# Kernel tuning notes

Hardware: AMD Instinct MI355X
Metric: run time of the kernel (lower is better)

## Reference

```python
import jax, jax.numpy as jnp
import numpy as np

NUM_GROUPS = 8
NUM_HEADS = 4
EPS = 1e-5


def group_norm(x, w, b):
    # x: [B, C, H, W]; normalize over (C/G, H, W) within each of G groups
    B, C, H, W = x.shape
    xg = x.reshape(B, NUM_GROUPS, C // NUM_GROUPS, H, W)
    mean = xg.mean(axis=(2, 3, 4), keepdims=True)
    var = xg.var(axis=(2, 3, 4), keepdims=True)
    xn = ((xg - mean) * jax.lax.rsqrt(var + EPS)).reshape(B, C, H, W)
    return xn * w[None, :, None, None] + b[None, :, None, None]


def setup_inputs() -> dict:
    key = jax.random.key(0)
    ks = jax.random.split(key, 7)
    B, C, H, W = 4, 256, 64, 64
    x = jax.random.normal(ks[0], (B, C, H, W), dtype=jnp.float32)
    gn_w = jax.random.normal(ks[1], (C,), dtype=jnp.float32) * 0.1 + 1.0
    gn_b = jax.random.normal(ks[2], (C,), dtype=jnp.float32) * 0.1
    qkv_w = jax.random.normal(ks[3], (3 * C, C), dtype=jnp.float32) / np.sqrt(C)
    qkv_b = jax.random.normal(ks[4], (3 * C,), dtype=jnp.float32) * 0.02
    proj_w = jax.random.normal(ks[5], (C, C), dtype=jnp.float32) / np.sqrt(C)
    proj_b = jax.random.normal(ks[6], (C,), dtype=jnp.float32) * 0.02
    return {"x": x, "gn_w": gn_w, "gn_b": gn_b, "qkv_w": qkv_w,
            "qkv_b": qkv_b, "proj_w": proj_w, "proj_b": proj_b}


def reference(x, gn_w, gn_b, qkv_w, qkv_b, proj_w, proj_b):
    B, C, H, W = x.shape
    nh = NUM_HEADS
    hd = C // nh
    scale = hd ** -0.5
    N = H * W

    h = group_norm(x, gn_w, gn_b)
    # 1x1 conv == channel matmul: [B, 3C, H, W]
    qkv = jnp.einsum('oc,bchw->bohw', qkv_w, h) + qkv_b[None, :, None, None]
    qkv = qkv.reshape(B, 3, nh, hd, N)  # matches torch .view(B,3,nh,hd,HW)
    q, k, v = qkv[:, 0], qkv[:, 1], qkv[:, 2]  # each [B, nh, hd, N]

    attn = jnp.einsum('bhdn,bhdm->bhnm', q, k) * scale  # [B, nh, N, N]
    attn = jax.nn.softmax(attn, axis=-1)
    out = jnp.einsum('bhnm,bhdm->bhdn', attn, v)  # [B, nh, hd, N]
    out = out.reshape(B, C, H, W)

    proj = jnp.einsum('oc,bchw->bohw', proj_w, out) + proj_b[None, :, None, None]
    return x + proj
```

## Files before the change

### kernel.cpp

```cpp
#include <hip/hip_runtime.h>
#include <hip/hip_bf16.h>

#define BB   4
#define CC   256
#define NN   4096
#define NH   4
#define HD   64
#define NG   8
#define GSZ  32
#define EPSV 1e-5f
#define SCALE_L2E 0.18033688f

typedef __bf16 bf16x8 __attribute__((ext_vector_type(8)));
typedef float  f32x4  __attribute__((ext_vector_type(4)));

#define MFMA16(a, b, c)  __builtin_amdgcn_mfma_f32_16x16x32_bf16((a), (b), (c), 0, 0, 0)

#if __has_builtin(__builtin_amdgcn_exp2f)
#define EXP2F __builtin_amdgcn_exp2f
#else
#define EXP2F exp2f
#endif

#define WAITV(n)  asm volatile("s_waitcnt vmcnt(" #n ")" ::: "memory")
#define WAITL0    asm volatile("s_waitcnt lgkmcnt(0)" ::: "memory")
#define SBAR      __builtin_amdgcn_s_barrier()
#define SCHED0    __builtin_amdgcn_sched_barrier(0)

__device__ inline unsigned short f2bf(float f) {
    unsigned int u = __float_as_uint(f);
    u += 0x7fffu + ((u >> 16) & 1u);
    return (unsigned short)(u >> 16);
}

__device__ __forceinline__ bf16x8 pk8(const f32x4& p0, const f32x4& p1) {
    alignas(16) unsigned int u[4];
    u[0] = __builtin_amdgcn_perm(__float_as_uint(p0[1]), __float_as_uint(p0[0]), 0x07060302u);
    u[1] = __builtin_amdgcn_perm(__float_as_uint(p0[3]), __float_as_uint(p0[2]), 0x07060302u);
    u[2] = __builtin_amdgcn_perm(__float_as_uint(p1[1]), __float_as_uint(p1[0]), 0x07060302u);
    u[3] = __builtin_amdgcn_perm(__float_as_uint(p1[3]), __float_as_uint(p1[2]), 0x07060302u);
    return *reinterpret_cast<bf16x8*>(u);
}

__device__ __forceinline__ void async_ld16(void* lds, const void* g) {
    __builtin_amdgcn_global_load_lds(
        (const __attribute__((address_space(1))) unsigned int*)g,
        (__attribute__((address_space(3))) unsigned int*)lds, 16, 0, 0);
}

__global__ void k_prep(const float* __restrict__ x, float* __restrict__ stats,
                       const float* __restrict__ wq, const float* __restrict__ wp,
                       unsigned short* __restrict__ oq, unsigned short* __restrict__ op) {
    int blk = blockIdx.x;
    int t = threadIdx.x;
    if (blk >= 256) {
        int i = (blk - 256) * 256 + t;
        if (i < 3 * CC * CC) oq[i] = f2bf(wq[i]);
        if (i < CC * CC)     op[i] = f2bf(wp[i]);
        return;
    }
    int b = blk >> 6, g = (blk >> 3) & 7, s = blk & 7;
    const float* p = x + ((size_t)(b * CC + g * GSZ)) * NN + s * 16384;
    float s0 = 0.f, s1 = 0.f;
    #pragma unroll
    for (int i = 0; i < 64; ++i) { float v = p[i * 256 + t]; s0 += v; s1 += v * v; }
    #pragma unroll
    for (int m = 1; m <= 32; m <<= 1) { s0 += __shfl_xor(s0, m); s1 += __shfl_xor(s1, m); }
    __shared__ float ls[8];
    int w = t >> 6;
    if ((t & 63) == 0) { ls[w * 2] = s0; ls[w * 2 + 1] = s1; }
    __syncthreads();
    if (t == 0) {
        float a0 = ls[0] + ls[2] + ls[4] + ls[6];
        float a1 = ls[1] + ls[3] + ls[5] + ls[7];
        atomicAdd(&stats[(b * NG + g) * 2 + 0], a0);
        atomicAdd(&stats[(b * NG + g) * 2 + 1], a1);
    }
}

__global__ void k_gnapply(const float* __restrict__ x, const float* __restrict__ gw,
                          const float* __restrict__ gb, const float* __restrict__ stats,
                          unsigned short* __restrict__ ht) {
    int b = blockIdx.z, ct = blockIdx.y, nt = blockIdx.x;
    int c0 = ct * 32, n0 = nt * 64;
    int t = threadIdx.x;
    __shared__ float tile[32][65];
    const float* xp = x + ((size_t)(b * CC + c0)) * NN + n0;
    int cl = t >> 6, nl = t & 63;
    #pragma unroll
    for (int p = 0; p < 8; ++p)
        tile[p * 4 + cl][nl] = xp[(size_t)(p * 4 + cl) * NN + nl];
    float sum = stats[(b * NG + ct) * 2 + 0];
    float ssq = stats[(b * NG + ct) * 2 + 1];
    float mean = sum * (1.0f / 131072.0f);
    float var  = ssq * (1.0f / 131072.0f) - mean * mean;
    float inv  = rsqrtf(var + EPSV);
    __syncthreads();
    int nw = t >> 2, ci = (t & 3) * 8;
    alignas(16) unsigned short o8[8];
    #pragma unroll
    for (int j = 0; j < 8; ++j) {
        int c = c0 + ci + j;
        float v = (tile[ci + j][nw] - mean) * inv * gw[c] + gb[c];
        o8[j] = f2bf(v);
    }
    *reinterpret_cast<uint4*>(ht + ((size_t)(b * NN + n0 + nw)) * CC + c0 + ci) =
        *reinterpret_cast<const uint4*>(o8);
}

__global__ void __launch_bounds__(256)
k_qkv(const unsigned short* __restrict__ ht, const unsigned short* __restrict__ wq,
      const float* __restrict__ qb,
      unsigned short* __restrict__ qt, unsigned short* __restrict__ kt,
      unsigned short* __restrict__ vt) {
    int bx = blockIdx.x, by = blockIdx.y;
    int t = threadIdx.x, wave = t >> 6, lane = t & 63;
    int l15 = lane & 15, quad = lane >> 4;
    int wm = wave >> 1, wn = wave & 1;

    __shared__ alignas(16) unsigned char smem[33792];

    const char* Ag = (const char*)wq + (size_t)by * 65536;
    const char* Bg = (const char*)ht + (size_t)bx * 65536;
    int row0 = t >> 2, slot = t & 3;
    size_t a0 = (size_t)row0 * 512 + slot * 16;
    size_t a1 = a0 + 64 * 512;
    unsigned int dst0 = wave * 1024;

    auto stage = [&](int buf, int kk) {
        size_t ko = (size_t)kk * 64;
        unsigned char* Ab = smem + buf * 8192;
        unsigned char* Bb = smem + 16384 + buf * 8192;
        async_ld16(Ab + dst0,        Ag + a0 + ko);
        async_ld16(Ab + 4096 + dst0, Ag + a1 + ko);
        async_ld16(Bb + dst0,        Bg + a0 + ko);
        async_ld16(Bb + 4096 + dst0, Bg + a1 + ko);
    };

    f32x4 acc[4][4];
    #pragma unroll
    for (int i = 0; i < 4; ++i)
        #pragma unroll
        for (int j = 0; j < 4; ++j) acc[i][j] = (f32x4){0.f, 0.f, 0.f, 0.f};

    stage(0, 0);
    stage(1, 1);

    for (int kk = 0; kk < 8; ++kk) {
        if (kk < 7) { WAITV(4); } else { WAITV(0); }
        SCHED0;
        SBAR;
        SCHED0;
        int cur = kk & 1;
        bf16x8 af[4], bf[4];
        #pragma unroll
        for (int f = 0; f < 4; ++f) {
            af[f] = *reinterpret_cast<const bf16x8*>(smem + cur * 8192 + (wm * 64 + f * 16 + l15) * 64 + quad * 16);
            bf[f] = *reinterpret_cast<const bf16x8*>(smem + 16384 + cur * 8192 + (wn * 64 + f * 16 + l15) * 64 + quad * 16);
        }
        #pragma unroll
        for (int fm = 0; fm < 4; ++fm)
            #pragma unroll
            for (int fn = 0; fn < 4; ++fn)
                acc[fm][fn] = MFMA16(af[fm], bf[fn], acc[fm][fn]);
        WAITL0;
        SCHED0;
        SBAR;
        SCHED0;
        if (kk < 6) stage(cur, kk + 2);
    }

    int s = by >> 1;
    int nn0 = bx * 128;
    int b = nn0 >> 12, nbase = nn0 & 4095;
    if (s < 2) {
        #pragma unroll
        for (int fm = 0; fm < 4; ++fm) {
            int o = by * 128 + wm * 64 + fm * 16 + quad * 4;
            int h = (o >> 6) & 3, d0 = o & 63;
            float bias[4];
            #pragma unroll
            for (int r = 0; r < 4; ++r) bias[r] = qb[o + r];
            #pragma unroll
            for (int fn = 0; fn < 4; ++fn) {
                int n = nbase + wn * 64 + fn * 16 + l15;
                alignas(8) unsigned short o4[4];
                if (s == 0) {
                    #pragma unroll
                    for (int r = 0; r < 4; ++r) o4[r] = f2bf((acc[fm][fn][r] + bias[r]) * SCALE_L2E);
                    *reinterpret_cast<uint2*>(qt + (((size_t)(b * NH + h) * NN) + n) * HD + d0) =
                        *reinterpret_cast<const uint2*>(o4);
                } else {
                    #pragma unroll
                    for (int r = 0; r < 4; ++r) o4[r] = f2bf(acc[fm][fn][r] + bias[r]);
                    *reinterpret_cast<uint2*>(kt + (((size_t)(b * NH + h) * NN) + n) * HD + d0) =
                        *reinterpret_cast<const uint2*>(o4);
                }
            }
        }
    } else {
        unsigned short* vtile = (unsigned short*)smem;
        #pragma unroll
        for (int fm = 0; fm < 4; ++fm) {
            int o  = by * 128 + wm * 64 + fm * 16 + quad * 4;
            int ol = wm * 64 + fm * 16 + quad * 4;
            float bias[4];
            #pragma unroll
            for (int r = 0; r < 4; ++r) bias[r] = qb[o + r];
            #pragma unroll
            for (int fn = 0; fn < 4; ++fn) {
                int nl = wn * 64 + fn * 16 + l15;
                #pragma unroll
                for (int r = 0; r < 4; ++r)
                    vtile[(ol + r) * 132 + nl] = f2bf(acc[fm][fn][r] + bias[r]);
            }
        }
        __syncthreads();
        int hbase = (by - 4) * 2;
        #pragma unroll
        for (int pass = 0; pass < 8; ++pass) {
            int row  = pass * 16 + (t >> 4);
            int col0 = (t & 15) * 8;
            int nb = (col0 & ~31) | ((col0 & 16) >> 1) | ((col0 & 8) >> 1);
            const unsigned short* src = vtile + row * 132 + nb;
            uint2 lo = *reinterpret_cast<const uint2*>(src);
            uint2 hi = *reinterpret_cast<const uint2*>(src + 16);
            uint4 o4 = make_uint4(lo.x, lo.y, hi.x, hi.y);
            int h = hbase + (row >> 6), d = row & 63;
            *reinterpret_cast<uint4*>(vt + ((size_t)(b * NH + h) * HD + d) * NN + nbase + col0) = o4;
        }
    }
}

__global__ void __launch_bounds__(256, 4)
k_attn(const unsigned short* __restrict__ qt, const unsigned short* __restrict__ kt,
       const unsigned short* __restrict__ vt,
       unsigned short* __restrict__ op0, unsigned short* __restrict__ op1,
       float* __restrict__ lip) {
    int bh = blockIdx.y;
    int split = blockIdx.z;
    int t = threadIdx.x, wave = t >> 6, lane = t & 63;
    int l15 = lane & 15, quad = lane >> 4;
    int qbase = blockIdx.x * 128 + wave * 32;
    int kbase = split * 2048;
    const unsigned short* qp = qt + (size_t)bh * NN * HD;
    const unsigned short* kp = kt + (size_t)bh * NN * HD;
    const unsigned short* vp = vt + (size_t)bh * HD * NN;

    __shared__ alignas(16) unsigned char kbuf[2][8192];
    __shared__ alignas(16) unsigned char vbuf[2][8192];

    int lr8 = lane >> 3, lc8 = lane & 7;
    int swz = lc8 ^ lr8;
    const char* ksrc = (const char*)kp + (size_t)(kbase + wave * 16 + lr8) * 128 + swz * 16;
    const char* vsrc = (const char*)vp + (size_t)(wave * 16 + lr8) * 8192 + (size_t)kbase * 2 + swz * 16;
    unsigned int dstw = wave * 2048;

    auto stage = [&](int buf) {
        async_ld16(kbuf[buf] + dstw,        ksrc);
        async_ld16(kbuf[buf] + dstw + 1024, ksrc + 1024);
        ksrc += 8192;
        async_ld16(vbuf[buf] + dstw,        vsrc);
        async_ld16(vbuf[buf] + dstw + 1024, vsrc + 8 * 8192);
        vsrc += 128;
    };

    bf16x8 qaA0 = *reinterpret_cast<const bf16x8*>(qp + (size_t)(qbase + l15) * HD + quad * 8);
    bf16x8 qaA1 = *reinterpret_cast<const bf16x8*>(qp + (size_t)(qbase + l15) * HD + 32 + quad * 8);
    bf16x8 qaB0 = *reinterpret_cast<const bf16x8*>(qp + (size_t)(qbase + 16 + l15) * HD + quad * 8);
    bf16x8 qaB1 = *reinterpret_cast<const bf16x8*>(qp + (size_t)(qbase + 16 + l15) * HD + 32 + quad * 8);

    const f32x4 Z4 = (f32x4){0.f, 0.f, 0.f, 0.f};
    bf16x8 vone;
    #pragma unroll
    for (int i = 0; i < 8; ++i) vone[i] = (__bf16)1.0f;

    f32x4 OA[4], OB[4];
    #pragma unroll
    for (int i = 0; i < 4; ++i) { OA[i] = Z4; OB[i] = Z4; }
    f32x4 liAA = Z4, liBB = Z4;

    int sx = l15 & 7;

    auto compute = [&](const unsigned char* kb, const unsigned char* vbb) {
        f32x4 sA0[2], sA1[2], sB0[2], sB1[2];
        __builtin_amdgcn_s_setprio(1);
        #pragma unroll
        for (int s = 0; s < 2; ++s) {
            int r0 = (s * 32 + l15) * 128;
            bf16x8 k00 = *reinterpret_cast<const bf16x8*>(kb + r0 + ((quad ^ sx) * 16));
            bf16x8 k01 = *reinterpret_cast<const bf16x8*>(kb + r0 + (((quad + 4) ^ sx) * 16));
            bf16x8 k10 = *reinterpret_cast<const bf16x8*>(kb + r0 + 2048 + ((quad ^ sx) * 16));
            bf16x8 k11 = *reinterpret_cast<const bf16x8*>(kb + r0 + 2048 + (((quad + 4) ^ sx) * 16));
            sA0[s] = MFMA16(k00, qaA0, Z4);  sA0[s] = MFMA16(k01, qaA1, sA0[s]);
            sA1[s] = MFMA16(k10, qaA0, Z4);  sA1[s] = MFMA16(k11, qaA1, sA1[s]);
            sB0[s] = MFMA16(k00, qaB0, Z4);  sB0[s] = MFMA16(k01, qaB1, sB0[s]);
            sB1[s] = MFMA16(k10, qaB0, Z4);  sB1[s] = MFMA16(k11, qaB1, sB1[s]);
        }
        __builtin_amdgcn_s_setprio(0);
        #pragma unroll
        for (int s = 0; s < 2; ++s) {
            f32x4 pA0, pA1, pB0, pB1;
            #pragma unroll
            for (int r = 0; r < 4; ++r) {
                pA0[r] = EXP2F(sA0[s][r]);  pA1[r] = EXP2F(sA1[s][r]);
                pB0[r] = EXP2F(sB0[s][r]);  pB1[r] = EXP2F(sB1[s][r]);
            }
            bf16x8 fA = pk8(pA0, pA1);
            bf16x8 fB = pk8(pB0, pB1);

            __builtin_amdgcn_s_setprio(1);
            liAA = MFMA16(fA, vone, liAA);
            liBB = MFMA16(fB, vone, liBB);

            #pragma unroll
            for (int dc = 0; dc < 4; ++dc) {
                const unsigned char* vrow = vbb + (dc * 16 + l15) * 128;
                bf16x8 vv = *reinterpret_cast<const bf16x8*>(vrow + (((s * 4 + quad) ^ sx) * 16));
                OA[dc] = MFMA16(fA, vv, OA[dc]);
                OB[dc] = MFMA16(fB, vv, OB[dc]);
            }
            __builtin_amdgcn_s_setprio(0);
        }
    };

    stage(0);
    __syncthreads();

    for (int p = 0; p < 16; ++p) {
        stage(1);
        compute(kbuf[0], vbuf[0]);
        __syncthreads();
        if (p < 15) stage(0);
        compute(kbuf[1], vbuf[1]);
        __syncthreads();
    }

    unsigned short* op = split ? op1 : op0;
    int b = bh >> 2, h = bh & 3;
    #pragma unroll
    for (int dc = 0; dc < 4; ++dc) {
        #pragma unroll
        for (int r = 0; r < 4; ++r) {
            int qA = qbase + quad * 4 + r;
            op[((size_t)(b * NN) + qA) * CC + h * HD + dc * 16 + l15]      = f2bf(OA[dc][r]);
            op[((size_t)(b * NN) + qA + 16) * CC + h * HD + dc * 16 + l15] = f2bf(OB[dc][r]);
        }
    }
    float* lp = lip + (size_t)split * (16 * NN) + (size_t)bh * NN + qbase;
    if (l15 == 0) {
        #pragma unroll
        for (int r = 0; r < 4; ++r) {
            lp[quad * 4 + r]      = liAA[r];
            lp[16 + quad * 4 + r] = liBB[r];
        }
    }
}

__global__ void __launch_bounds__(256)
k_proj(const unsigned short* __restrict__ ao, const unsigned short* __restrict__ p1,
       const float* __restrict__ lip,
       const unsigned short* __restrict__ wp, const float* __restrict__ pb,
       const float* __restrict__ x, float* __restrict__ out) {
    int bx = blockIdx.x, by = blockIdx.y;
    int t = threadIdx.x, wave = t >> 6, lane = t & 63;
    int l15 = lane & 15, quad = lane >> 4;
    int wm = wave >> 1, wn = wave & 1;

    __shared__ alignas(16) unsigned char At[2][4096];
    __shared__ alignas(16) unsigned char Bt[2][4096];

    const char* Ag = (const char*)wp + (size_t)by * 32768;
    int row0 = t >> 2, slot = t & 3;
    size_t a0 = (size_t)row0 * 512 + slot * 16;
    unsigned int dst0 = wave * 1024;

    int gtok = bx * 64 + row0;
    int b = gtok >> 12, n = gtok & 4095;
    size_t obase = ((size_t)(b * NN) + n) * CC + slot * 8;
    float inv[4];
    #pragma unroll
    for (int h = 0; h < 4; ++h) {
        size_t lb = (size_t)(b * 4 + h) * NN + n;
        inv[h] = 1.0f / (lip[lb] + lip[lb + (size_t)16 * NN]);
    }

    auto stageA = [&](int buf, int kk) {
        async_ld16(At[buf] + dst0, Ag + a0 + (size_t)kk * 64);
    };
    uint4 eu0, eu1, ou0, ou1;
    auto loadB = [&](uint4& r0, uint4& r1, int kk) {
        r0 = *reinterpret_cast<const uint4*>(ao + obase + kk * 32);
        r1 = *reinterpret_cast<const uint4*>(p1 + obase + kk * 32);
    };
    auto writeB = [&](int buf, const uint4& r0, const uint4& r1, float iv) {
        const unsigned short* q0 = reinterpret_cast<const unsigned short*>(&r0);
        const unsigned short* q1 = reinterpret_cast<const unsigned short*>(&r1);
        alignas(16) unsigned short o8[8];
        #pragma unroll
        for (int i = 0; i < 8; ++i) {
            float f0 = __uint_as_float((unsigned)q0[i] << 16);
            float f1 = __uint_as_float((unsigned)q1[i] << 16);
            o8[i] = f2bf((f0 + f1) * iv);
        }
        *reinterpret_cast<uint4*>(Bt[buf] + row0 * 64 + slot * 16) =
            *reinterpret_cast<const uint4*>(o8);
    };

    f32x4 acc[2][2];
    #pragma unroll
    for (int i = 0; i < 2; ++i)
        #pragma unroll
        for (int j = 0; j < 2; ++j) acc[i][j] = (f32x4){0.f, 0.f, 0.f, 0.f};

    loadB(eu0, eu1, 0);
    stageA(0, 0);
    loadB(ou0, ou1, 1);

    #pragma unroll
    for (int k2 = 0; k2 < 4; ++k2) {
        {
            const int kk = 2 * k2;
            WAITV(2);
            SCHED0;
            writeB(0, eu0, eu1, inv[kk >> 1]);
            WAITL0;
            SCHED0;
            SBAR;
            SCHED0;
            if (kk < 7) stageA(1, kk + 1);
            if (kk < 6) loadB(eu0, eu1, kk + 2);
            bf16x8 af[2], bf[2];
            #pragma unroll
            for (int f = 0; f < 2; ++f) {
                af[f] = *reinterpret_cast<const bf16x8*>(At[0] + (wm * 32 + f * 16 + l15) * 64 + quad * 16);
                bf[f] = *reinterpret_cast<const bf16x8*>(Bt[0] + (wn * 32 + f * 16 + l15) * 64 + quad * 16);
            }
            #pragma unroll
            for (int fm = 0; fm < 2; ++fm)
                #pragma unroll
                for (int fn = 0; fn < 2; ++fn)
                    acc[fm][fn] = MFMA16(af[fm], bf[fn], acc[fm][fn]);
        }
        {
            const int kk = 2 * k2 + 1;
            if (kk < 7) { WAITV(2); } else { WAITV(0); }
            SCHED0;
            writeB(1, ou0, ou1, inv[kk >> 1]);
            WAITL0;
            SCHED0;
            SBAR;
            SCHED0;
            if (kk < 7) stageA(0, kk + 1);
            if (kk < 6) loadB(ou0, ou1, kk + 2);
            bf16x8 af[2], bf[2];
            #pragma unroll
            for (int f = 0; f < 2; ++f) {
                af[f] = *reinterpret_cast<const bf16x8*>(At[1] + (wm * 32 + f * 16 + l15) * 64 + quad * 16);
                bf[f] = *reinterpret_cast<const bf16x8*>(Bt[1] + (wn * 32 + f * 16 + l15) * 64 + quad * 16);
            }
            #pragma unroll
            for (int fm = 0; fm < 2; ++fm)
                #pragma unroll
                for (int fn = 0; fn < 2; ++fn)
                    acc[fm][fn] = MFMA16(af[fm], bf[fn], acc[fm][fn]);
        }
    }

    int nn0 = bx * 64;
    int bb = nn0 >> 12, nbase = nn0 & 4095;
    #pragma unroll
    for (int fm = 0; fm < 2; ++fm) {
        int o = by * 64 + wm * 32 + fm * 16 + quad * 4;
        float bias[4];
        #pragma unroll
        for (int r = 0; r < 4; ++r) bias[r] = pb[o + r];
        #pragma unroll
        for (int fn = 0; fn < 2; ++fn) {
            int nc = nbase + wn * 32 + fn * 16 + l15;
            #pragma unroll
            for (int r = 0; r < 4; ++r) {
                size_t idx = ((size_t)(bb * CC + o + r)) * NN + nc;
                out[idx] = acc[fm][fn][r] + bias[r] + x[idx];
            }
        }
    }
}

extern "C" void kernel_launch(void* const* d_in, const int* in_sizes, int n_in,
                              void* d_out, int out_size, void* d_ws, size_t ws_size,
                              hipStream_t stream) {
    const float* x     = (const float*)d_in[0];
    const float* gw    = (const float*)d_in[1];
    const float* gb    = (const float*)d_in[2];
    const float* qkvw  = (const float*)d_in[3];
    const float* qkvb  = (const float*)d_in[4];
    const float* projw = (const float*)d_in[5];
    const float* projb = (const float*)d_in[6];
    float* out = (float*)d_out;

    char* w = (char*)d_ws;
    size_t off = 0;
    unsigned short* ht = (unsigned short*)(w + off); off += (size_t)BB * NN * CC * 2;
    unsigned short* qt = (unsigned short*)(w + off); off += (size_t)BB * NH * NN * HD * 2;
    unsigned short* kt = (unsigned short*)(w + off); off += (size_t)BB * NH * NN * HD * 2;
    unsigned short* vt = (unsigned short*)(w + off); off += (size_t)BB * NH * HD * NN * 2;
    unsigned short* ao = (unsigned short*)(w + off); off += (size_t)BB * NN * CC * 2;
    unsigned short* wqb = (unsigned short*)(w + off); off += (size_t)3 * CC * CC * 2;
    unsigned short* wpb = (unsigned short*)(w + off); off += (size_t)CC * CC * 2;
    float* stats = (float*)(w + off); off += BB * NG * 2 * sizeof(float);
    float* lip   = (float*)(w + off); off += (size_t)2 * 16 * NN * sizeof(float);

    hipMemsetAsync(stats, 0, BB * NG * 2 * sizeof(float), stream);
    k_prep<<<1024, 256, 0, stream>>>(x, stats, qkvw, projw, wqb, wpb);
    k_gnapply<<<dim3(NN / 64, CC / 32, BB), 256, 0, stream>>>(x, gw, gb, stats, ht);
    k_qkv<<<dim3(BB * NN / 128, 6), 256, 0, stream>>>(ht, wqb, qkvb, qt, kt, vt);
    k_attn<<<dim3(NN / 128, BB * NH, 2), 256, 0, stream>>>(qt, kt, vt, ao, ht, lip);
    k_proj<<<dim3(BB * NN / 64, CC / 64), 256, 0, stream>>>(ao, ht, lip, wpb, projb, x, out);
}
```

Measured before the change: 186.0 us.

## Fold GroupNorm into per-batch QKV weights and read raw x in GEMM

Removes the separate GroupNorm-apply kernel and its bf16 intermediate. The per-channel scale is folded into a per-batch scaled copy of the QKV weight, and the shift is folded into a per-batch bias through a small table kernel. The QKV GEMM now streams fp32 x directly into LDS and converts to bf16 while forming fragments. This saves a full activation write and read, at the cost of twice the B-operand LDS traffic, extra convert instructions in the inner loop, and per-batch weight tables.

```diff
diff --git a/kernel.cpp b/kernel.cpp
--- a/kernel.cpp
+++ b/kernel.cpp
@@ -49,14 +49,12 @@
 }
 
 __global__ void k_prep(const float* __restrict__ x, float* __restrict__ stats,
-                       const float* __restrict__ wq, const float* __restrict__ wp,
-                       unsigned short* __restrict__ oq, unsigned short* __restrict__ op) {
+                       const float* __restrict__ wp, unsigned short* __restrict__ op) {
     int blk = blockIdx.x;
     int t = threadIdx.x;
     if (blk >= 256) {
         int i = (blk - 256) * 256 + t;
-        if (i < 3 * CC * CC) oq[i] = f2bf(wq[i]);
-        if (i < CC * CC)     op[i] = f2bf(wp[i]);
+        if (i < CC * CC) op[i] = f2bf(wp[i]);
         return;
     }
     int b = blk >> 6, g = (blk >> 3) & 7, s = blk & 7;
@@ -78,39 +76,32 @@
     }
 }
 
-__global__ void k_gnapply(const float* __restrict__ x, const float* __restrict__ gw,
-                          const float* __restrict__ gb, const float* __restrict__ stats,
-                          unsigned short* __restrict__ ht) {
-    int b = blockIdx.z, ct = blockIdx.y, nt = blockIdx.x;
-    int c0 = ct * 32, n0 = nt * 64;
-    int t = threadIdx.x;
-    __shared__ float tile[32][65];
-    const float* xp = x + ((size_t)(b * CC + c0)) * NN + n0;
-    int cl = t >> 6, nl = t & 63;
-    #pragma unroll
-    for (int p = 0; p < 8; ++p)
-        tile[p * 4 + cl][nl] = xp[(size_t)(p * 4 + cl) * NN + nl];
-    float sum = stats[(b * NG + ct) * 2 + 0];
-    float ssq = stats[(b * NG + ct) * 2 + 1];
-    float mean = sum * (1.0f / 131072.0f);
-    float var  = ssq * (1.0f / 131072.0f) - mean * mean;
+__global__ void __launch_bounds__(256)
+k_tab(const float* __restrict__ wq, const float* __restrict__ gw, const float* __restrict__ gb,
+      const float* __restrict__ qb, const float* __restrict__ stats,
+      unsigned short* __restrict__ wqp, float* __restrict__ biasq) {
+    int o = blockIdx.x, b = blockIdx.y, c = threadIdx.x;
+    float s0 = stats[(b * NG + (c >> 5)) * 2 + 0];
+    float s1 = stats[(b * NG + (c >> 5)) * 2 + 1];
+    float mean = s0 * (1.0f / 131072.0f);
+    float var  = s1 * (1.0f / 131072.0f) - mean * mean;
     float inv  = rsqrtf(var + EPSV);
+    float Ac = gw[c] * inv;
+    float Bc = gb[c] - mean * Ac;
+    float w = wq[o * CC + c];
+    wqp[((size_t)b * 768 + o) * CC + c] = f2bf(w * Ac);
+    float p = w * Bc;
+    #pragma unroll
+    for (int m = 1; m <= 32; m <<= 1) p += __shfl_xor(p, m);
+    __shared__ float ls[4];
+    if ((c & 63) == 0) ls[c >> 6] = p;
     __syncthreads();
-    int nw = t >> 2, ci = (t & 3) * 8;
-    alignas(16) unsigned short o8[8];
-    #pragma unroll
-    for (int j = 0; j < 8; ++j) {
-        int c = c0 + ci + j;
-        float v = (tile[ci + j][nw] - mean) * inv * gw[c] + gb[c];
-        o8[j] = f2bf(v);
-    }
-    *reinterpret_cast<uint4*>(ht + ((size_t)(b * NN + n0 + nw)) * CC + c0 + ci) =
-        *reinterpret_cast<const uint4*>(o8);
+    if (c == 0) biasq[b * 768 + o] = qb[o] + ls[0] + ls[1] + ls[2] + ls[3];
 }
 
 __global__ void __launch_bounds__(256)
-k_qkv(const unsigned short* __restrict__ ht, const unsigned short* __restrict__ wq,
-      const float* __restrict__ qb,
+k_qkv(const float* __restrict__ x, const unsigned short* __restrict__ wqp,
+      const float* __restrict__ biasq,
       unsigned short* __restrict__ qt, unsigned short* __restrict__ kt,
       unsigned short* __restrict__ vt) {
     int bx = blockIdx.x, by = blockIdx.y;
@@ -118,24 +109,36 @@
     int l15 = lane & 15, quad = lane >> 4;
     int wm = wave >> 1, wn = wave & 1;
 
-    __shared__ alignas(16) unsigned char smem[33792];
-
-    const char* Ag = (const char*)wq + (size_t)by * 65536;
-    const char* Bg = (const char*)ht + (size_t)bx * 65536;
+    __shared__ alignas(16) unsigned char smem[49152];
+
+    int nn0 = bx * 128;
+    int b = nn0 >> 12, nbase = nn0 & 4095;
+
+    const char* Ag = (const char*)wqp + (size_t)b * 393216 + (size_t)by * 65536;
     int row0 = t >> 2, slot = t & 3;
     size_t a0 = (size_t)row0 * 512 + slot * 16;
     size_t a1 = a0 + 64 * 512;
-    unsigned int dst0 = wave * 1024;
+    unsigned int dstA = wave * 1024;
+
+    int colsrc = (((lane & 31) * 16) - 32 * wave) & 511;
+    const char* xrow = (const char*)x +
+        (((size_t)(b * CC) + (wave * 8 + (lane >> 5))) * NN + nbase) * 4 + colsrc;
 
     auto stage = [&](int buf, int kk) {
-        size_t ko = (size_t)kk * 64;
-        unsigned char* Ab = smem + buf * 8192;
-        unsigned char* Bb = smem + 16384 + buf * 8192;
-        async_ld16(Ab + dst0,        Ag + a0 + ko);
-        async_ld16(Ab + 4096 + dst0, Ag + a1 + ko);
-        async_ld16(Bb + dst0,        Bg + a0 + ko);
-        async_ld16(Bb + 4096 + dst0, Bg + a1 + ko);
+        async_ld16(smem + buf * 8192 + dstA,        Ag + a0 + (size_t)kk * 64);
+        async_ld16(smem + buf * 8192 + 4096 + dstA, Ag + a1 + (size_t)kk * 64);
+        const char* bs = xrow + (size_t)kk * 32 * NN * 4;
+        unsigned char* bd = smem + 16384 + buf * 16384 + wave * 4096;
+        async_ld16(bd,        bs);
+        async_ld16(bd + 1024, bs + (size_t)2 * NN * 4);
+        async_ld16(bd + 2048, bs + (size_t)4 * NN * 4);
+        async_ld16(bd + 3072, bs + (size_t)6 * NN * 4);
     };
+
+    int colr[4];
+    #pragma unroll
+    for (int f = 0; f < 4; ++f)
+        colr[f] = (((wn * 64 + f * 16 + l15) * 4) + quad * 32) & 511;
 
     f32x4 acc[4][4];
     #pragma unroll
@@ -147,16 +150,26 @@
     stage(1, 1);
 
     for (int kk = 0; kk < 8; ++kk) {
-        if (kk < 7) { WAITV(4); } else { WAITV(0); }
+        if (kk < 7) { WAITV(6); } else { WAITV(0); }
         SCHED0;
         SBAR;
         SCHED0;
         int cur = kk & 1;
         bf16x8 af[4], bf[4];
         #pragma unroll
+        for (int f = 0; f < 4; ++f)
+            af[f] = *reinterpret_cast<const bf16x8*>(smem + cur * 8192 + (wm * 64 + f * 16 + l15) * 64 + quad * 16);
+        #pragma unroll
         for (int f = 0; f < 4; ++f) {
-            af[f] = *reinterpret_cast<const bf16x8*>(smem + cur * 8192 + (wm * 64 + f * 16 + l15) * 64 + quad * 16);
-            bf[f] = *reinterpret_cast<const bf16x8*>(smem + 16384 + cur * 8192 + (wn * 64 + f * 16 + l15) * 64 + quad * 16);
+            const unsigned char* fb = smem + 16384 + cur * 16384 + quad * 4096 + colr[f];
+            alignas(16) unsigned int u[4];
+            #pragma unroll
+            for (int jj = 0; jj < 4; ++jj) {
+                float xl = *reinterpret_cast<const float*>(fb + (2 * jj) * 512);
+                float xh = *reinterpret_cast<const float*>(fb + (2 * jj + 1) * 512);
+                asm("v_cvt_pk_bf16_f32 %0, %1, %2" : "=v"(u[jj]) : "v"(xl), "v"(xh));
+            }
+            bf[f] = *reinterpret_cast<const bf16x8*>(u);
         }
         #pragma unroll
         for (int fm = 0; fm < 4; ++fm)
@@ -171,8 +184,6 @@
     }
 
     int s = by >> 1;
-    int nn0 = bx * 128;
-    int b = nn0 >> 12, nbase = nn0 & 4095;
     if (s < 2) {
         #pragma unroll
         for (int fm = 0; fm < 4; ++fm) {
@@ -180,7 +191,7 @@
             int h = (o >> 6) & 3, d0 = o & 63;
             float bias[4];
             #pragma unroll
-            for (int r = 0; r < 4; ++r) bias[r] = qb[o + r];
+            for (int r = 0; r < 4; ++r) bias[r] = biasq[b * 768 + o + r];
             #pragma unroll
             for (int fn = 0; fn < 4; ++fn) {
                 int n = nbase + wn * 64 + fn * 16 + l15;
@@ -206,7 +217,7 @@
             int ol = wm * 64 + fm * 16 + quad * 4;
             float bias[4];
             #pragma unroll
-            for (int r = 0; r < 4; ++r) bias[r] = qb[o + r];
+            for (int r = 0; r < 4; ++r) bias[r] = biasq[b * 768 + o + r];
             #pragma unroll
             for (int fn = 0; fn < 4; ++fn) {
                 int nl = wn * 64 + fn * 16 + l15;
@@ -501,20 +512,21 @@
 
     char* w = (char*)d_ws;
     size_t off = 0;
-    unsigned short* ht = (unsigned short*)(w + off); off += (size_t)BB * NN * CC * 2;
     unsigned short* qt = (unsigned short*)(w + off); off += (size_t)BB * NH * NN * HD * 2;
     unsigned short* kt = (unsigned short*)(w + off); off += (size_t)BB * NH * NN * HD * 2;
     unsigned short* vt = (unsigned short*)(w + off); off += (size_t)BB * NH * HD * NN * 2;
     unsigned short* ao = (unsigned short*)(w + off); off += (size_t)BB * NN * CC * 2;
-    unsigned short* wqb = (unsigned short*)(w + off); off += (size_t)3 * CC * CC * 2;
+    unsigned short* pt1 = (unsigned short*)(w + off); off += (size_t)BB * NN * CC * 2;
+    unsigned short* wqp = (unsigned short*)(w + off); off += (size_t)BB * 3 * CC * CC * 2;
+    float* biasq = (float*)(w + off); off += (size_t)BB * 3 * CC * sizeof(float);
     unsigned short* wpb = (unsigned short*)(w + off); off += (size_t)CC * CC * 2;
     float* stats = (float*)(w + off); off += BB * NG * 2 * sizeof(float);
     float* lip   = (float*)(w + off); off += (size_t)2 * 16 * NN * sizeof(float);
 
     hipMemsetAsync(stats, 0, BB * NG * 2 * sizeof(float), stream);
-    k_prep<<<1024, 256, 0, stream>>>(x, stats, qkvw, projw, wqb, wpb);
-    k_gnapply<<<dim3(NN / 64, CC / 32, BB), 256, 0, stream>>>(x, gw, gb, stats, ht);
-    k_qkv<<<dim3(BB * NN / 128, 6), 256, 0, stream>>>(ht, wqb, qkvb, qt, kt, vt);
-    k_attn<<<dim3(NN / 128, BB * NH, 2), 256, 0, stream>>>(qt, kt, vt, ao, ht, lip);
-    k_proj<<<dim3(BB * NN / 64, CC / 64), 256, 0, stream>>>(ao, ht, lip, wpb, projb, x, out);
-}
+    k_prep<<<512, 256, 0, stream>>>(x, stats, projw, wpb);
+    k_tab<<<dim3(3 * CC, BB), 256, 0, stream>>>(qkvw, gw, gb, qkvb, stats, wqp, biasq);
+    k_qkv<<<dim3(BB * NN / 128, 6), 256, 0, stream>>>(x, wqp, biasq, qt, kt, vt);
+    k_attn<<<dim3(NN / 128, BB * NH, 2), 256, 0, stream>>>(qt, kt, vt, ao, pt1, lip);
+    k_proj<<<dim3(BB * NN / 64, CC / 64), 256, 0, stream>>>(ao, pt1, lip, wpb, projb, x, out);
+}
```

After: 185.4 us. About the same (-0.3%).
